# Optimization experiments

Measured on AMD Instinct MI355X. Metric: run time of the kernel, lower is better.

The kernel has to match this reference:

```python
import jax, jax.numpy as jnp
import numpy as np

B, N, S, VOCAB, D, NNZ = 16, 2048, 4096, 50257, 128, 1048576


def setup_inputs() -> dict:
    key = jax.random.key(0)
    k1, k2, k3, k4, k5, k6 = jax.random.split(key, 6)
    return {
        "subnode_ids": jax.random.randint(k1, (B, S), 0, VOCAB),
        "mask_batch": jax.random.randint(k2, (NNZ,), 0, B),
        "mask_node": jax.random.randint(k3, (NNZ,), 0, N),
        "mask_subnode": jax.random.randint(k4, (NNZ,), 0, S),
        "mask_values": jax.random.uniform(k5, (NNZ,), dtype=jnp.float32),
        "emb_table": jax.random.normal(k6, (VOCAB, D), dtype=jnp.float32),
    }


def reference(subnode_ids, mask_batch, mask_node, mask_subnode, mask_values, emb_table):
    # Gather token embeddings for every (batch, subnode) slot: [B, S, D] -> [B*S, D]
    subnode_emb = emb_table[subnode_ids].reshape(B * S, D)
    # Flattened COO indices (same as batch*max_nodes + node, batch*max_subnodes + subnode)
    row = mask_batch * N + mask_node      # destination node slot in [0, B*N)
    col = mask_batch * S + mask_subnode   # source subnode slot in [0, B*S)
    # Fused gather + weighted scatter-add (== sparse.mm of expanded_mask @ subnode_emb)
    contrib = subnode_emb[col] * mask_values[:, None]           # [NNZ, D]
    pooled = jax.ops.segment_sum(contrib, row, num_segments=B * N)  # [B*N, D]
    return pooled.reshape(B, N, D)
```

## Files before the change

kernel.cpp:

```cpp
#include <hip/hip_runtime.h>
#include <hip/hip_fp16.h>

#define Bq 16
#define Nq 2048
#define Sq 4096
#define Dq 128
#define VOCABq 50257
#define NNZq 1048576
#define ROWS (Bq * Nq)
#define NBIN 512
#define RPB 64
#define BTPB 512
#define BEPT 4
#define ENT (BTPB * BEPT)
#define NBBLK (NNZq / ENT)
#define PTPB 1024
#define NKEY 256
#define EBUF 2560

typedef unsigned long long u64;
typedef u64 u64x2 __attribute__((ext_vector_type(2)));
typedef float vfloat4 __attribute__((ext_vector_type(4)));
typedef unsigned short vushort4 __attribute__((ext_vector_type(4)));
typedef unsigned short vushort8 __attribute__((ext_vector_type(8)));

__global__ __launch_bounds__(256) void cast_kernel(
    const float* __restrict__ emb, unsigned short* __restrict__ emb16)
{
    const int NQUAD = (VOCABq * Dq) / 4;
    int i = blockIdx.x * 256 + threadIdx.x;
    if (i >= NQUAD) return;
    vfloat4 f = reinterpret_cast<const vfloat4*>(emb)[i];
    vushort4 h;
    h.x = __half_as_ushort(__float2half_rn(f.x));
    h.y = __half_as_ushort(__float2half_rn(f.y));
    h.z = __half_as_ushort(__float2half_rn(f.z));
    h.w = __half_as_ushort(__float2half_rn(f.w));
    __builtin_nontemporal_store(h, reinterpret_cast<vushort4*>(emb16) + i);
}

__global__ __launch_bounds__(BTPB) void bin_kernel(
    const int* __restrict__ subnode_ids,
    const int* __restrict__ mb,
    const int* __restrict__ mn,
    const int* __restrict__ ms,
    const float* __restrict__ mv,
    u64* __restrict__ binMem,
    int* __restrict__ offTab)
{
    __shared__ int hist[NBIN];
    __shared__ int lstart[NBIN];
    __shared__ int waveSum[BTPB / 64];
    __shared__ u64 spk[ENT] __attribute__((aligned(16)));

    int t = threadIdx.x;
    hist[t] = 0;
    __syncthreads();

    int blockBase = blockIdx.x * ENT;
    int g[BEPT], rank[BEPT];
    u64 pk[BEPT];
    #pragma unroll
    for (int k = 0; k < BEPT; k++) {
        int i   = blockBase + k * BTPB + t;
        int b   = __builtin_nontemporal_load(mb + i);
        int row = b * Nq + __builtin_nontemporal_load(mn + i);
        int s   = __builtin_nontemporal_load(ms + i);
        float v = __builtin_nontemporal_load(mv + i);
        int tok = subnode_ids[b * Sq + s];
        g[k]  = row >> 6;
        pk[k] = ((u64)(unsigned)__float_as_int(v) << 32)
              | ((u64)(row & 63) << 16)
              | (unsigned)tok;
        rank[k] = atomicAdd(&hist[g[k]], 1);
    }
    __syncthreads();

    int lane = t & 63, wid = t >> 6;
    int v  = hist[t];
    int vi = v;
    #pragma unroll
    for (int d = 1; d < 64; d <<= 1) {
        int w = __shfl_up(vi, d, 64);
        if (lane >= d) vi += w;
    }
    if (lane == 63) waveSum[wid] = vi;
    __syncthreads();
    if (t == 0) {
        int s = 0;
        #pragma unroll
        for (int w = 0; w < BTPB / 64; w++) { int x = waveSum[w]; waveSum[w] = s; s += x; }
    }
    __syncthreads();
    int ex = vi - v + waveSum[wid];
    lstart[t] = ex;
    offTab[blockIdx.x * NBIN + t] = ex;
    __syncthreads();

    #pragma unroll
    for (int k = 0; k < BEPT; k++)
        spk[lstart[g[k]] + rank[k]] = pk[k];
    __syncthreads();

    const u64x2* s2 = reinterpret_cast<const u64x2*>(spk);
    u64x2* d2 = reinterpret_cast<u64x2*>(binMem + (size_t)blockIdx.x * ENT);
    #pragma unroll
    for (int p = t; p < ENT / 2; p += BTPB)
        d2[p] = s2[p];
}

__global__ __launch_bounds__(PTPB) void pool_kernel(
    const unsigned short* __restrict__ emb16,
    const u64* __restrict__ binMem,
    const int* __restrict__ offTab,
    float* __restrict__ out)
{
    __shared__ u64 ebuf[EBUF];
    __shared__ int hist[NKEY];
    __shared__ int start[NKEY + 1];
    __shared__ int cursor[NKEY];
    __shared__ int waveSum[NKEY / 64];
    __shared__ int sstart[NBBLK];
    __shared__ int scnt[NBBLK];

    int t   = threadIdx.x;
    int bin = blockIdx.x;
    if (t < NKEY) hist[t] = 0;
    __syncthreads();

    if (t < NBBLK) {
        int s0 = offTab[t * NBIN + bin];
        int s1 = (bin == NBIN - 1) ? ENT : offTab[t * NBIN + bin + 1];
        sstart[t] = s0;
        scnt[t]   = s1 - s0;
        const u64* src = binMem + (size_t)t * ENT;
        for (int e = s0; e < s1; e++) {
            u64 pk  = src[e];
            int tok = (int)(pk & 0xFFFF);
            int key = ((tok >> 14) << 6) | (int)((pk >> 16) & 63);
            atomicAdd(&hist[key], 1);
        }
    }
    __syncthreads();

    int lane = t & 63, wid = t >> 6;
    int v  = (t < NKEY) ? hist[t] : 0;
    int vi = v;
    #pragma unroll
    for (int d = 1; d < 64; d <<= 1) {
        int w = __shfl_up(vi, d, 64);
        if (lane >= d) vi += w;
    }
    if (t < NKEY && lane == 63) waveSum[wid] = vi;
    __syncthreads();
    if (t == 0) {
        int s = 0;
        #pragma unroll
        for (int w = 0; w < NKEY / 64; w++) { int x = waveSum[w]; waveSum[w] = s; s += x; }
    }
    __syncthreads();
    if (t < NKEY) {
        int ex = vi - v + waveSum[wid];
        start[t]  = ex;
        cursor[t] = ex;
        if (t == NKEY - 1) start[NKEY] = ex + v;
    }
    __syncthreads();

    if (t < NBBLK) {
        const u64* src = binMem + (size_t)t * ENT + sstart[t];
        int c = scnt[t];
        for (int e = 0; e < c; e++) {
            u64 pk  = src[e];
            int tok = (int)(pk & 0xFFFF);
            int key = ((tok >> 14) << 6) | (int)((pk >> 16) & 63);
            int p = atomicAdd(&cursor[key], 1);
            if (p < EBUF) ebuf[p] = pk;
        }
    }
    __syncthreads();

    int g      = t >> 4;
    int lane16 = t & 15;
    vfloat4 a0 = {0.f, 0.f, 0.f, 0.f};
    vfloat4 a1 = {0.f, 0.f, 0.f, 0.f};
    #pragma unroll
    for (int q = 0; q < 4; q++) {
        int s0 = min(start[q * 64 + g], EBUF);
        int s1 = min(start[q * 64 + g + 1], EBUF);
        int k = s0;
        for (; k + 8 <= s1; k += 8) {
            int   tk[8];
            float vv[8];
            #pragma unroll
            for (int u = 0; u < 8; u++) {
                u64 pk = ebuf[k + u];
                tk[u] = (int)(pk & 0xFFFF);
                vv[u] = __int_as_float((int)(pk >> 32));
            }
            vushort8 e[8];
            #pragma unroll
            for (int u = 0; u < 8; u++)
                e[u] = reinterpret_cast<const vushort8*>(emb16 + (size_t)tk[u] * Dq)[lane16];
            #pragma unroll
            for (int u = 0; u < 8; u++) {
                a0.x += __half2float(__ushort_as_half(e[u][0])) * vv[u];
                a0.y += __half2float(__ushort_as_half(e[u][1])) * vv[u];
                a0.z += __half2float(__ushort_as_half(e[u][2])) * vv[u];
                a0.w += __half2float(__ushort_as_half(e[u][3])) * vv[u];
                a1.x += __half2float(__ushort_as_half(e[u][4])) * vv[u];
                a1.y += __half2float(__ushort_as_half(e[u][5])) * vv[u];
                a1.z += __half2float(__ushort_as_half(e[u][6])) * vv[u];
                a1.w += __half2float(__ushort_as_half(e[u][7])) * vv[u];
            }
        }
        for (; k < s1; k++) {
            u64 pk = ebuf[k];
            int   tok = (int)(pk & 0xFFFF);
            float v2  = __int_as_float((int)(pk >> 32));
            vushort8 e = reinterpret_cast<const vushort8*>(emb16 + (size_t)tok * Dq)[lane16];
            a0.x += __half2float(__ushort_as_half(e[0])) * v2;
            a0.y += __half2float(__ushort_as_half(e[1])) * v2;
            a0.z += __half2float(__ushort_as_half(e[2])) * v2;
            a0.w += __half2float(__ushort_as_half(e[3])) * v2;
            a1.x += __half2float(__ushort_as_half(e[4])) * v2;
            a1.y += __half2float(__ushort_as_half(e[5])) * v2;
            a1.z += __half2float(__ushort_as_half(e[6])) * v2;
            a1.w += __half2float(__ushort_as_half(e[7])) * v2;
        }
    }

    float* orow = out + ((size_t)bin * RPB + g) * Dq + lane16 * 8;
    __builtin_nontemporal_store(a0, reinterpret_cast<vfloat4*>(orow));
    __builtin_nontemporal_store(a1, reinterpret_cast<vfloat4*>(orow) + 1);
}

extern "C" void kernel_launch(void* const* d_in, const int* in_sizes, int n_in,
                              void* d_out, int out_size, void* d_ws, size_t ws_size,
                              hipStream_t stream) {
    const int*   subnode_ids  = (const int*)d_in[0];
    const int*   mask_batch   = (const int*)d_in[1];
    const int*   mask_node    = (const int*)d_in[2];
    const int*   mask_subnode = (const int*)d_in[3];
    const float* mask_values  = (const float*)d_in[4];
    const float* emb_table    = (const float*)d_in[5];
    float*       out          = (float*)d_out;

    unsigned short* emb16 = (unsigned short*)d_ws;
    u64* binMem = (u64*)(emb16 + (size_t)VOCABq * Dq + 64 );
    int* offTab = (int*)(binMem + (size_t)NBBLK * ENT);

    const int NQUAD = (VOCABq * Dq) / 4;
    cast_kernel<<<(NQUAD + 255) / 256, 256, 0, stream>>>(emb_table, emb16);
    bin_kernel<<<NBBLK, BTPB, 0, stream>>>(
        subnode_ids, mask_batch, mask_node, mask_subnode, mask_values,
        binMem, offTab);
    pool_kernel<<<NBIN, PTPB, 0, stream>>>(emb16, binMem, offTab, out);
}
```

Baseline: 138.6 us.

## Restructure pool kernel: staged segment load, parallel key sort, two rows per thread

The bin kernel now packs per-bin start and count into offTab, so the pool kernel no longer has to re-read neighbouring offsets. The pool kernel drops to 512 threads: each thread copies its source segment into shared memory, then histogram and scatter run across all threads instead of serial per-block loops over global memory read twice. Each 16-lane group accumulates two output rows, which halves thread count and raises per-thread gather work. Overflow beyond EBUF is truncated as before, and occupancy and latency hiding shift.

```diff
diff --git a/kernel.cpp b/kernel.cpp
--- a/kernel.cpp
+++ b/kernel.cpp
@@ -10,13 +10,13 @@
 #define ROWS (Bq * Nq)
 #define NBIN 512
 #define RPB 64
-#define BTPB 512
+#define TPB 512
 #define BEPT 4
-#define ENT (BTPB * BEPT)
-#define NBBLK (NNZq / ENT)
-#define PTPB 1024
+#define ENT (TPB * BEPT)
+#define NBLK (NNZq / ENT)
 #define NKEY 256
 #define EBUF 2560
+#define NQUAD ((VOCABq * Dq) / 4)
 
 typedef unsigned long long u64;
 typedef u64 u64x2 __attribute__((ext_vector_type(2)));
@@ -24,10 +24,73 @@
 typedef unsigned short vushort4 __attribute__((ext_vector_type(4)));
 typedef unsigned short vushort8 __attribute__((ext_vector_type(8)));
 
+__device__ __forceinline__ int scan_block(int val, int t, int* waveSum) {
+    int lane = t & 63, wid = t >> 6;
+    int vi = val;
+    #pragma unroll
+    for (int d = 1; d < 64; d <<= 1) {
+        int w = __shfl_up(vi, d, 64);
+        if (lane >= d) vi += w;
+    }
+    if (lane == 63) waveSum[wid] = vi;
+    __syncthreads();
+    if (t == 0) {
+        int s = 0;
+        #pragma unroll
+        for (int w = 0; w < TPB / 64; w++) { int x = waveSum[w]; waveSum[w] = s; s += x; }
+    }
+    __syncthreads();
+    return vi - val + waveSum[wid];
+}
+
+__device__ __forceinline__ void accum_range(
+    const u64* ebuf, int s0, int s1, int lane16,
+    const unsigned short* __restrict__ emb16, vfloat4& A0, vfloat4& A1)
+{
+    int k = s0;
+    for (; k + 8 <= s1; k += 8) {
+        int tk[8]; float vv[8];
+        #pragma unroll
+        for (int u = 0; u < 8; u++) {
+            u64 pk = ebuf[k + u];
+            tk[u] = (int)(pk & 0xFFFF);
+            vv[u] = __int_as_float((int)(pk >> 32));
+        }
+        vushort8 e[8];
+        #pragma unroll
+        for (int u = 0; u < 8; u++)
+            e[u] = reinterpret_cast<const vushort8*>(emb16 + (size_t)tk[u] * Dq)[lane16];
+        #pragma unroll
+        for (int u = 0; u < 8; u++) {
+            A0.x += __half2float(__ushort_as_half(e[u][0])) * vv[u];
+            A0.y += __half2float(__ushort_as_half(e[u][1])) * vv[u];
+            A0.z += __half2float(__ushort_as_half(e[u][2])) * vv[u];
+            A0.w += __half2float(__ushort_as_half(e[u][3])) * vv[u];
+            A1.x += __half2float(__ushort_as_half(e[u][4])) * vv[u];
+            A1.y += __half2float(__ushort_as_half(e[u][5])) * vv[u];
+            A1.z += __half2float(__ushort_as_half(e[u][6])) * vv[u];
+            A1.w += __half2float(__ushort_as_half(e[u][7])) * vv[u];
+        }
+    }
+    for (; k < s1; k++) {
+        u64 pk = ebuf[k];
+        int   tok = (int)(pk & 0xFFFF);
+        float v2  = __int_as_float((int)(pk >> 32));
+        vushort8 e = reinterpret_cast<const vushort8*>(emb16 + (size_t)tok * Dq)[lane16];
+        A0.x += __half2float(__ushort_as_half(e[0])) * v2;
+        A0.y += __half2float(__ushort_as_half(e[1])) * v2;
+        A0.z += __half2float(__ushort_as_half(e[2])) * v2;
+        A0.w += __half2float(__ushort_as_half(e[3])) * v2;
+        A1.x += __half2float(__ushort_as_half(e[4])) * v2;
+        A1.y += __half2float(__ushort_as_half(e[5])) * v2;
+        A1.z += __half2float(__ushort_as_half(e[6])) * v2;
+        A1.w += __half2float(__ushort_as_half(e[7])) * v2;
+    }
+}
+
 __global__ __launch_bounds__(256) void cast_kernel(
     const float* __restrict__ emb, unsigned short* __restrict__ emb16)
 {
-    const int NQUAD = (VOCABq * Dq) / 4;
     int i = blockIdx.x * 256 + threadIdx.x;
     if (i >= NQUAD) return;
     vfloat4 f = reinterpret_cast<const vfloat4*>(emb)[i];
@@ -39,30 +102,32 @@
     __builtin_nontemporal_store(h, reinterpret_cast<vushort4*>(emb16) + i);
 }
 
-__global__ __launch_bounds__(BTPB) void bin_kernel(
+__global__ __launch_bounds__(TPB) void bin_kernel(
     const int* __restrict__ subnode_ids,
     const int* __restrict__ mb,
     const int* __restrict__ mn,
     const int* __restrict__ ms,
     const float* __restrict__ mv,
     u64* __restrict__ binMem,
-    int* __restrict__ offTab)
+    unsigned* __restrict__ offTab)
 {
     __shared__ int hist[NBIN];
     __shared__ int lstart[NBIN];
-    __shared__ int waveSum[BTPB / 64];
+    __shared__ int waveSum[TPB / 64];
     __shared__ u64 spk[ENT] __attribute__((aligned(16)));
 
-    int t = threadIdx.x;
+    int t   = threadIdx.x;
+    int blk = blockIdx.x;
+
     hist[t] = 0;
     __syncthreads();
 
-    int blockBase = blockIdx.x * ENT;
+    int base = blk * ENT;
     int g[BEPT], rank[BEPT];
     u64 pk[BEPT];
     #pragma unroll
     for (int k = 0; k < BEPT; k++) {
-        int i   = blockBase + k * BTPB + t;
+        int i   = base + k * TPB + t;
         int b   = __builtin_nontemporal_load(mb + i);
         int row = b * Nq + __builtin_nontemporal_load(mn + i);
         int s   = __builtin_nontemporal_load(ms + i);
@@ -76,25 +141,10 @@
     }
     __syncthreads();
 
-    int lane = t & 63, wid = t >> 6;
-    int v  = hist[t];
-    int vi = v;
-    #pragma unroll
-    for (int d = 1; d < 64; d <<= 1) {
-        int w = __shfl_up(vi, d, 64);
-        if (lane >= d) vi += w;
-    }
-    if (lane == 63) waveSum[wid] = vi;
-    __syncthreads();
-    if (t == 0) {
-        int s = 0;
-        #pragma unroll
-        for (int w = 0; w < BTPB / 64; w++) { int x = waveSum[w]; waveSum[w] = s; s += x; }
-    }
-    __syncthreads();
-    int ex = vi - v + waveSum[wid];
+    int cnt = hist[t];
+    int ex  = scan_block(cnt, t, waveSum);
     lstart[t] = ex;
-    offTab[blockIdx.x * NBIN + t] = ex;
+    offTab[blk * NBIN + t] = (unsigned)ex | ((unsigned)cnt << 16);
     __syncthreads();
 
     #pragma unroll
@@ -103,136 +153,86 @@
     __syncthreads();
 
     const u64x2* s2 = reinterpret_cast<const u64x2*>(spk);
-    u64x2* d2 = reinterpret_cast<u64x2*>(binMem + (size_t)blockIdx.x * ENT);
-    #pragma unroll
-    for (int p = t; p < ENT / 2; p += BTPB)
-        d2[p] = s2[p];
-}
-
-__global__ __launch_bounds__(PTPB) void pool_kernel(
+    u64x2* d2 = reinterpret_cast<u64x2*>(binMem + (size_t)blk * ENT);
+    #pragma unroll
+    for (int p = t; p < ENT / 2; p += TPB) d2[p] = s2[p];
+}
+
+__global__ __launch_bounds__(TPB) void pool_kernel(
     const unsigned short* __restrict__ emb16,
     const u64* __restrict__ binMem,
-    const int* __restrict__ offTab,
+    const unsigned* __restrict__ offTab,
     float* __restrict__ out)
 {
+    __shared__ u64 spk[EBUF] __attribute__((aligned(16)));
     __shared__ u64 ebuf[EBUF];
-    __shared__ int hist[NKEY];
-    __shared__ int start[NKEY + 1];
-    __shared__ int cursor[NKEY];
-    __shared__ int waveSum[NKEY / 64];
-    __shared__ int sstart[NBBLK];
-    __shared__ int scnt[NBBLK];
+    __shared__ int waveSum[TPB / 64];
+    __shared__ int khist[NKEY];
+    __shared__ int kstart[NKEY + 1];
+    __shared__ int kcursor[NKEY];
+    __shared__ int nTot;
 
     int t   = threadIdx.x;
     int bin = blockIdx.x;
-    if (t < NKEY) hist[t] = 0;
-    __syncthreads();
-
-    if (t < NBBLK) {
-        int s0 = offTab[t * NBIN + bin];
-        int s1 = (bin == NBIN - 1) ? ENT : offTab[t * NBIN + bin + 1];
-        sstart[t] = s0;
-        scnt[t]   = s1 - s0;
-        const u64* src = binMem + (size_t)t * ENT;
-        for (int e = s0; e < s1; e++) {
-            u64 pk  = src[e];
-            int tok = (int)(pk & 0xFFFF);
-            int key = ((tok >> 14) << 6) | (int)((pk >> 16) & 63);
-            atomicAdd(&hist[key], 1);
-        }
-    }
-    __syncthreads();
-
-    int lane = t & 63, wid = t >> 6;
-    int v  = (t < NKEY) ? hist[t] : 0;
-    int vi = v;
-    #pragma unroll
-    for (int d = 1; d < 64; d <<= 1) {
-        int w = __shfl_up(vi, d, 64);
-        if (lane >= d) vi += w;
-    }
-    if (t < NKEY && lane == 63) waveSum[wid] = vi;
-    __syncthreads();
-    if (t == 0) {
-        int s = 0;
-        #pragma unroll
-        for (int w = 0; w < NKEY / 64; w++) { int x = waveSum[w]; waveSum[w] = s; s += x; }
-    }
-    __syncthreads();
+
+    unsigned m = offTab[t * NBIN + bin];
+    int soff = (int)(m & 0xFFFFu);
+    int scnt = (int)(m >> 16);
+    int db   = scan_block(scnt, t, waveSum);
+    if (t == TPB - 1) nTot = db + scnt;
+    if (db >= EBUF) scnt = 0;
+    else if (db + scnt > EBUF) scnt = EBUF - db;
+
+    {
+        const u64* src = binMem + (size_t)t * ENT + soff;
+        for (int i = 0; i < scnt; i++) spk[db + i] = src[i];
+    }
+    if (t < NKEY) khist[t] = 0;
+    __syncthreads();
+
+    int n = nTot < EBUF ? nTot : EBUF;
+
+    for (int e = t; e < n; e += TPB) {
+        u64 p = spk[e];
+        int key = (((int)(p & 0xFFFF)) >> 14 << 6) | ((int)(p >> 16) & 63);
+        atomicAdd(&khist[key], 1);
+    }
+    __syncthreads();
+
+    int kval = (t < NKEY) ? khist[t] : 0;
+    int kex  = scan_block(kval, t, waveSum);
     if (t < NKEY) {
-        int ex = vi - v + waveSum[wid];
-        start[t]  = ex;
-        cursor[t] = ex;
-        if (t == NKEY - 1) start[NKEY] = ex + v;
-    }
-    __syncthreads();
-
-    if (t < NBBLK) {
-        const u64* src = binMem + (size_t)t * ENT + sstart[t];
-        int c = scnt[t];
-        for (int e = 0; e < c; e++) {
-            u64 pk  = src[e];
-            int tok = (int)(pk & 0xFFFF);
-            int key = ((tok >> 14) << 6) | (int)((pk >> 16) & 63);
-            int p = atomicAdd(&cursor[key], 1);
-            if (p < EBUF) ebuf[p] = pk;
-        }
-    }
-    __syncthreads();
-
-    int g      = t >> 4;
+        kstart[t]  = kex;
+        kcursor[t] = kex;
+        if (t == NKEY - 1) kstart[NKEY] = kex + kval;
+    }
+    __syncthreads();
+
+    for (int e = t; e < n; e += TPB) {
+        u64 p = spk[e];
+        int key = (((int)(p & 0xFFFF)) >> 14 << 6) | ((int)(p >> 16) & 63);
+        int pos = atomicAdd(&kcursor[key], 1);
+        ebuf[pos] = p;
+    }
+    __syncthreads();
+
+    int g2     = t >> 4;
     int lane16 = t & 15;
-    vfloat4 a0 = {0.f, 0.f, 0.f, 0.f};
-    vfloat4 a1 = {0.f, 0.f, 0.f, 0.f};
+    int r0 = g2, r1 = g2 + 32;
+    vfloat4 a0 = {0.f,0.f,0.f,0.f}, a1 = {0.f,0.f,0.f,0.f};
+    vfloat4 b0 = {0.f,0.f,0.f,0.f}, b1 = {0.f,0.f,0.f,0.f};
     #pragma unroll
     for (int q = 0; q < 4; q++) {
-        int s0 = min(start[q * 64 + g], EBUF);
-        int s1 = min(start[q * 64 + g + 1], EBUF);
-        int k = s0;
-        for (; k + 8 <= s1; k += 8) {
-            int   tk[8];
-            float vv[8];
-            #pragma unroll
-            for (int u = 0; u < 8; u++) {
-                u64 pk = ebuf[k + u];
-                tk[u] = (int)(pk & 0xFFFF);
-                vv[u] = __int_as_float((int)(pk >> 32));
-            }
-            vushort8 e[8];
-            #pragma unroll
-            for (int u = 0; u < 8; u++)
-                e[u] = reinterpret_cast<const vushort8*>(emb16 + (size_t)tk[u] * Dq)[lane16];
-            #pragma unroll
-            for (int u = 0; u < 8; u++) {
-                a0.x += __half2float(__ushort_as_half(e[u][0])) * vv[u];
-                a0.y += __half2float(__ushort_as_half(e[u][1])) * vv[u];
-                a0.z += __half2float(__ushort_as_half(e[u][2])) * vv[u];
-                a0.w += __half2float(__ushort_as_half(e[u][3])) * vv[u];
-                a1.x += __half2float(__ushort_as_half(e[u][4])) * vv[u];
-                a1.y += __half2float(__ushort_as_half(e[u][5])) * vv[u];
-                a1.z += __half2float(__ushort_as_half(e[u][6])) * vv[u];
-                a1.w += __half2float(__ushort_as_half(e[u][7])) * vv[u];
-            }
-        }
-        for (; k < s1; k++) {
-            u64 pk = ebuf[k];
-            int   tok = (int)(pk & 0xFFFF);
-            float v2  = __int_as_float((int)(pk >> 32));
-            vushort8 e = reinterpret_cast<const vushort8*>(emb16 + (size_t)tok * Dq)[lane16];
-            a0.x += __half2float(__ushort_as_half(e[0])) * v2;
-            a0.y += __half2float(__ushort_as_half(e[1])) * v2;
-            a0.z += __half2float(__ushort_as_half(e[2])) * v2;
-            a0.w += __half2float(__ushort_as_half(e[3])) * v2;
-            a1.x += __half2float(__ushort_as_half(e[4])) * v2;
-            a1.y += __half2float(__ushort_as_half(e[5])) * v2;
-            a1.z += __half2float(__ushort_as_half(e[6])) * v2;
-            a1.w += __half2float(__ushort_as_half(e[7])) * v2;
-        }
-    }
-
-    float* orow = out + ((size_t)bin * RPB + g) * Dq + lane16 * 8;
-    __builtin_nontemporal_store(a0, reinterpret_cast<vfloat4*>(orow));
-    __builtin_nontemporal_store(a1, reinterpret_cast<vfloat4*>(orow) + 1);
+        accum_range(ebuf, kstart[q * 64 + r0], kstart[q * 64 + r0 + 1], lane16, emb16, a0, a1);
+        accum_range(ebuf, kstart[q * 64 + r1], kstart[q * 64 + r1 + 1], lane16, emb16, b0, b1);
+    }
+
+    float* orow0 = out + ((size_t)bin * RPB + r0) * Dq + lane16 * 8;
+    float* orow1 = out + ((size_t)bin * RPB + r1) * Dq + lane16 * 8;
+    __builtin_nontemporal_store(a0, reinterpret_cast<vfloat4*>(orow0));
+    __builtin_nontemporal_store(a1, reinterpret_cast<vfloat4*>(orow0) + 1);
+    __builtin_nontemporal_store(b0, reinterpret_cast<vfloat4*>(orow1));
+    __builtin_nontemporal_store(b1, reinterpret_cast<vfloat4*>(orow1) + 1);
 }
 
 extern "C" void kernel_launch(void* const* d_in, const int* in_sizes, int n_in,
@@ -248,12 +248,11 @@
 
     unsigned short* emb16 = (unsigned short*)d_ws;
     u64* binMem = (u64*)(emb16 + (size_t)VOCABq * Dq + 64 );
-    int* offTab = (int*)(binMem + (size_t)NBBLK * ENT);
-
-    const int NQUAD = (VOCABq * Dq) / 4;
+    unsigned* offTab = (unsigned*)(binMem + (size_t)NBLK * ENT);
+
     cast_kernel<<<(NQUAD + 255) / 256, 256, 0, stream>>>(emb_table, emb16);
-    bin_kernel<<<NBBLK, BTPB, 0, stream>>>(
+    bin_kernel<<<NBLK, TPB, 0, stream>>>(
         subnode_ids, mask_batch, mask_node, mask_subnode, mask_values,
         binMem, offTab);
-    pool_kernel<<<NBIN, PTPB, 0, stream>>>(emb16, binMem, offTab, out);
-}
+    pool_kernel<<<NBIN, TPB, 0, stream>>>(emb16, binMem, offTab, out);
+}
```

Result: faster. 135.8 us (-2.0%).
